# Performance work log

Hardware: AMD Instinct MI355X
Metric: run time of the kernel (lower is better)

Reference implementation:

```python
import jax, jax.numpy as jnp
import numpy as np

N_NODES = 100000
N_EDGES = 1600000
D_IN = 128
D_OUT = 128


def setup_inputs() -> dict:
    key = jax.random.key(0)
    k_x, k_s, k_r, k_w = jax.random.split(key, 4)
    x = jax.random.normal(k_x, (N_NODES, D_IN), dtype=jnp.float32)
    senders = jax.random.randint(k_s, (N_EDGES,), 0, N_NODES, dtype=jnp.int32)
    receivers = jax.random.randint(k_r, (N_EDGES,), 0, N_NODES, dtype=jnp.int32)
    # xavier_uniform for (D_IN, D_OUT)
    limit = float(np.sqrt(6.0 / (D_IN + D_OUT)))
    weight = jax.random.uniform(k_w, (D_IN, D_OUT), dtype=jnp.float32,
                                minval=-limit, maxval=limit)
    bias = jnp.zeros((D_OUT,), dtype=jnp.float32)
    return {"x": x, "senders": senders, "receivers": receivers,
            "n_node": N_NODES, "weight": weight, "bias": bias}


def reference(x, senders, receivers, n_node, weight, bias):
    # Linear node update: [N, D_in] @ [D_in, D_out] + bias
    h = jnp.dot(x, weight) + bias
    total_num_nodes = x.shape[0]

    # Degree counts via segment_sum of ones (symmetric normalization)
    ones = jnp.ones_like(senders)
    sender_degree = jax.ops.segment_sum(ones, senders, num_segments=total_num_nodes)
    receiver_degree = jax.ops.segment_sum(ones, receivers, num_segments=total_num_nodes)

    # Pre-scale by 1/sqrt(deg_out), scatter-sum along edges, post-scale by 1/sqrt(deg_in)
    h = h * jax.lax.rsqrt(jnp.maximum(sender_degree, 1.0))[:, None]
    agg = jax.ops.segment_sum(h[senders], receivers, num_segments=total_num_nodes)
    out = agg * jax.lax.rsqrt(jnp.maximum(receiver_degree, 1.0))[:, None]
    return out
```

## Files before the change

kernel.cpp:

```cpp
#include <hip/hip_runtime.h>
#include <hip/hip_bf16.h>
#include <stdint.h>

#define N_NODES 100000
#define N_EDGES 1600000
#define TILE 8192
#define NB 196
#define BIN_BLOCKS ((N_EDGES + TILE - 1) / TILE)

static const size_t OFF_H      = 0;
static const size_t OFF_SSCALE = 25600000;
static const size_t OFF_ROWP   = 26000000;
static const size_t OFF_RHIST  = 26400016;
static const size_t OFF_SHIST  = 26401040;
static const size_t OFF_RBASE  = 26402064;
static const size_t OFF_SBASE  = 26403088;
static const size_t OFF_RCUR   = 26404112;
static const size_t OFF_SCUR   = 26405136;
static const size_t OFF_EBUF   = 26406160;
static const size_t OFF_SBUF   = 32806160;

using short8 = __attribute__((ext_vector_type(8))) short;
using f32x4  = __attribute__((ext_vector_type(4))) float;

static __device__ __forceinline__ short f2bf(float f) {
    uint32_t u = __float_as_uint(f);
    uint32_t r = (u + 0x7fffu + ((u >> 16) & 1u)) >> 16;
    return (short)r;
}

__global__ __launch_bounds__(256) void hist196_kernel(const int* __restrict__ snd,
                                                      const int* __restrict__ rcv,
                                                      int* __restrict__ rhist,
                                                      int* __restrict__ shist) {
    __shared__ int hr[256], hs[256];
    int t = threadIdx.x;
    hr[t] = 0; hs[t] = 0;
    __syncthreads();
    int base = blockIdx.x * TILE;
    #pragma unroll
    for (int j = 0; j < 32; j++) {
        int idx = base + j * 256 + t;
        if (idx < N_EDGES) {
            atomicAdd(&hr[rcv[idx] >> 9], 1);
            atomicAdd(&hs[snd[idx] >> 9], 1);
        }
    }
    __syncthreads();
    if (t < NB) {
        if (hr[t]) atomicAdd(&rhist[t], hr[t]);
        if (hs[t]) atomicAdd(&shist[t], hs[t]);
    }
}

__global__ __launch_bounds__(256) void scanb_kernel(const int* __restrict__ rhist,
                                                    const int* __restrict__ shist,
                                                    int* __restrict__ rbase,
                                                    int* __restrict__ sbase,
                                                    int* __restrict__ rcur,
                                                    int* __restrict__ scur,
                                                    int* __restrict__ row_ptr) {
    __shared__ int s[256];
    int t = threadIdx.x;

    int v = (t < NB) ? rhist[t] : 0;
    s[t] = v;
    __syncthreads();
    #pragma unroll
    for (int off = 1; off < 256; off <<= 1) {
        int tv = (t >= off) ? s[t - off] : 0;
        __syncthreads();
        s[t] += tv;
        __syncthreads();
    }
    if (t < NB) { int e = s[t] - v; rbase[t] = e; rcur[t] = e; }
    __syncthreads();

    v = (t < NB) ? shist[t] : 0;
    s[t] = v;
    __syncthreads();
    #pragma unroll
    for (int off = 1; off < 256; off <<= 1) {
        int tv = (t >= off) ? s[t - off] : 0;
        __syncthreads();
        s[t] += tv;
        __syncthreads();
    }
    if (t < NB) { int e = s[t] - v; sbase[t] = e; scur[t] = e; }
    if (t == 0) row_ptr[N_NODES] = N_EDGES;
}

__global__ __launch_bounds__(256) void binr_kernel(const int* __restrict__ snd,
                                                   const int* __restrict__ rcv,
                                                   int* __restrict__ rcur,
                                                   int* __restrict__ scur,
                                                   uint32_t* __restrict__ ebuf,
                                                   uint16_t* __restrict__ sbuf) {
    __shared__ int hist[256];
    __shared__ int coff[256];
    __shared__ int ccur[256];
    __shared__ int gbase[256];
    __shared__ uint32_t stage[TILE];

    const int t = threadIdx.x;
    const int base = blockIdx.x * TILE;

    uint32_t ss[32], rs[32];
    #pragma unroll
    for (int j = 0; j < 32; j++) {
        int idx = base + j * 256 + t;
        bool ok = idx < N_EDGES;
        ss[j] = ok ? (uint32_t)snd[idx] : 0u;
        rs[j] = ok ? (uint32_t)rcv[idx] : 0xffffffffu;
    }

    hist[t] = 0;
    __syncthreads();
    #pragma unroll
    for (int j = 0; j < 32; j++)
        if (rs[j] != 0xffffffffu) atomicAdd(&hist[rs[j] >> 9], 1);
    __syncthreads();

    int v = hist[t];
    ccur[t] = v;
    __syncthreads();
    #pragma unroll
    for (int off = 1; off < 256; off <<= 1) {
        int tv = (t >= off) ? ccur[t - off] : 0;
        __syncthreads();
        ccur[t] += tv;
        __syncthreads();
    }
    int excl = ccur[t] - v;
    coff[t] = excl;
    int gb = 0;
    if (v > 0) gb = atomicAdd(&rcur[t], v);
    gbase[t] = gb - excl;
    __syncthreads();
    ccur[t] = excl;
    __syncthreads();

    #pragma unroll
    for (int j = 0; j < 32; j++) {
        uint32_t r = rs[j];
        if (r != 0xffffffffu) {
            int pos = atomicAdd(&ccur[r >> 9], 1);
            stage[pos] = (ss[j] << 9) | (r & 511u);
        }
    }
    __syncthreads();

    int total = coff[255] + hist[255];
    for (int i = t; i < total; i += 256) {
        uint32_t pv = stage[i];
        int lo = 0;
        #pragma unroll
        for (int step = 128; step; step >>= 1)
            if (lo + step < 256 && coff[lo + step] <= i) lo += step;
        ebuf[gbase[lo] + i] = pv;
    }
    __syncthreads();

    hist[t] = 0;
    __syncthreads();
    #pragma unroll
    for (int j = 0; j < 32; j++)
        if (rs[j] != 0xffffffffu) atomicAdd(&hist[ss[j] >> 9], 1);
    __syncthreads();

    v = hist[t];
    ccur[t] = v;
    __syncthreads();
    #pragma unroll
    for (int off = 1; off < 256; off <<= 1) {
        int tv = (t >= off) ? ccur[t - off] : 0;
        __syncthreads();
        ccur[t] += tv;
        __syncthreads();
    }
    excl = ccur[t] - v;
    coff[t] = excl;
    gb = 0;
    if (v > 0) gb = atomicAdd(&scur[t], v);
    gbase[t] = gb - excl;
    __syncthreads();
    ccur[t] = excl;
    __syncthreads();

    uint16_t* stage16 = (uint16_t*)stage;
    #pragma unroll
    for (int j = 0; j < 32; j++) {
        if (rs[j] != 0xffffffffu) {
            int pos = atomicAdd(&ccur[ss[j] >> 9], 1);
            stage16[pos] = (uint16_t)(ss[j] & 511u);
        }
    }
    __syncthreads();

    total = coff[255] + hist[255];
    for (int i = t; i < total; i += 256) {
        uint16_t pv = stage16[i];
        int lo = 0;
        #pragma unroll
        for (int step = 128; step; step >>= 1)
            if (lo + step < 256 && coff[lo + step] <= i) lo += step;
        sbuf[gbase[lo] + i] = pv;
    }
}

__global__ __launch_bounds__(256) void bucket_kernel(const int* __restrict__ rbase,
                                                     const int* __restrict__ rhist,
                                                     const int* __restrict__ sbase,
                                                     const int* __restrict__ shist,
                                                     uint32_t* __restrict__ ebuf,
                                                     const uint16_t* __restrict__ sbuf,
                                                     int* __restrict__ row_ptr,
                                                     float* __restrict__ sscale) {
    __shared__ int hist_l[512];
    __shared__ int excl_l[512];
    __shared__ int cur_l[512];
    __shared__ int ps[256];
    __shared__ uint32_t inb[9216];
    __shared__ uint32_t perm[9216];

    const int b = blockIdx.x;
    const int t = threadIdx.x;
    const int nbase = b << 9;
    const int base = rbase[b];
    const int size = rhist[b];

    hist_l[t] = 0; hist_l[t + 256] = 0;
    __syncthreads();

    for (int i = t; i < size; i += 256) {
        uint32_t v = ebuf[base + i];
        inb[i] = v;
        atomicAdd(&hist_l[v & 511u], 1);
    }
    __syncthreads();

    int h0 = hist_l[2 * t], h1 = hist_l[2 * t + 1];
    int p = h0 + h1;
    ps[t] = p;
    __syncthreads();
    #pragma unroll
    for (int off = 1; off < 256; off <<= 1) {
        int tv = (t >= off) ? ps[t - off] : 0;
        __syncthreads();
        ps[t] += tv;
        __syncthreads();
    }
    int pe = ps[t] - p;
    excl_l[2 * t] = pe;
    excl_l[2 * t + 1] = pe + h0;
    cur_l[2 * t] = pe;
    cur_l[2 * t + 1] = pe + h0;
    __syncthreads();

    for (int i = t; i < 512; i += 256) {
        int n = nbase + i;
        if (n < N_NODES) row_ptr[n] = base + excl_l[i];
    }

    for (int i = t; i < size; i += 256) {
        uint32_t v = inb[i];
        int pos = atomicAdd(&cur_l[v & 511u], 1);
        perm[pos] = v >> 9;
    }
    __syncthreads();
    for (int i = t; i < size; i += 256)
        ebuf[base + i] = perm[i];

    __syncthreads();
    hist_l[t] = 0; hist_l[t + 256] = 0;
    __syncthreads();
    const int sb = sbase[b];
    const int ssz = shist[b];
    for (int i = t; i < ssz; i += 256)
        atomicAdd(&hist_l[(int)sbuf[sb + i]], 1);
    __syncthreads();
    for (int i = t; i < 512; i += 256) {
        int n = nbase + i;
        if (n < N_NODES) sscale[n] = rsqrtf(fmaxf((float)hist_l[i], 1.f));
    }
}

__global__ __launch_bounds__(256) void gemm_mfma_kernel(const float* __restrict__ x,
                                                        const float* __restrict__ W,
                                                        const float* __restrict__ bias,
                                                        const float* __restrict__ sscale,
                                                        short* __restrict__ h) {
    __shared__ __align__(16) short Wl[32 * 64 * 8];
    __shared__ float bias_s[128];

    const int t = threadIdx.x;
    const int lane = t & 63;
    const int wv = t >> 6;
    const int quad = lane >> 4;
    const int mcol = lane & 15;

    #pragma unroll
    for (int i = 0; i < 8; i++) {
        int f = wv + 4 * i;
        int s = f >> 3;
        int c = f & 7;
        int krow = s * 32 + quad * 8;
        int ncol = c * 16 + mcol;
        short8 wf;
        #pragma unroll
        for (int j = 0; j < 8; j++)
            wf[j] = f2bf(W[(krow + j) * 128 + ncol]);
        *(short8*)&Wl[(f * 64 + lane) * 8] = wf;
    }
    if (t < 128) bias_s[t] = bias[t];

    const int node0 = blockIdx.x * 128 + wv * 32;
    short8 afrag[2][4];
    #pragma unroll
    for (int mf = 0; mf < 2; mf++) {
        int node = node0 + mf * 16 + mcol;
        bool ok = node < N_NODES;
        const float* xr = x + (size_t)(ok ? node : 0) * 128;
        #pragma unroll
        for (int s = 0; s < 4; s++) {
            int k0 = s * 32 + quad * 8;
            f32x4 v0 = ok ? *(const f32x4*)(xr + k0)     : f32x4{0.f,0.f,0.f,0.f};
            f32x4 v1 = ok ? *(const f32x4*)(xr + k0 + 4) : f32x4{0.f,0.f,0.f,0.f};
            short8 af;
            #pragma unroll
            for (int j = 0; j < 4; j++) {
                af[j]     = f2bf(v0[j]);
                af[4 + j] = f2bf(v1[j]);
            }
            afrag[mf][s] = af;
        }
    }

    __syncthreads();

    f32x4 acc[2][8];
    #pragma unroll
    for (int mf = 0; mf < 2; mf++)
        #pragma unroll
        for (int c = 0; c < 8; c++)
            acc[mf][c] = f32x4{0.f, 0.f, 0.f, 0.f};

    #pragma unroll
    for (int s = 0; s < 4; s++) {
        #pragma unroll
        for (int c = 0; c < 8; c++) {
            short8 bfrag = *(const short8*)&Wl[((s * 8 + c) * 64 + lane) * 8];
            acc[0][c] = __builtin_amdgcn_mfma_f32_16x16x32_bf16(afrag[0][s], bfrag, acc[0][c], 0, 0, 0);
            acc[1][c] = __builtin_amdgcn_mfma_f32_16x16x32_bf16(afrag[1][s], bfrag, acc[1][c], 0, 0, 0);
        }
    }

    float rsv[2][4];
    #pragma unroll
    for (int mf = 0; mf < 2; mf++)
        #pragma unroll
        for (int r = 0; r < 4; r++) {
            int nd = node0 + mf * 16 + quad * 4 + r;
            rsv[mf][r] = (nd < N_NODES) ? sscale[nd] : 1.f;
        }

    #pragma unroll
    for (int mf = 0; mf < 2; mf++)
        #pragma unroll
        for (int c = 0; c < 8; c++) {
            float bval = bias_s[c * 16 + mcol];
            #pragma unroll
            for (int r = 0; r < 4; r++) {
                int nd = node0 + mf * 16 + quad * 4 + r;
                if (nd < N_NODES)
                    h[(size_t)nd * 128 + c * 16 + mcol] =
                        f2bf((acc[mf][c][r] + bval) * rsv[mf][r]);
            }
        }
}

__global__ __launch_bounds__(256) void gather_kernel(const uint32_t* __restrict__ h2,
                                                     const int* __restrict__ row_ptr,
                                                     const uint32_t* __restrict__ esrc,
                                                     float2* __restrict__ out2) {
    int node = blockIdx.x * 4 + (threadIdx.x >> 6);
    int lane = threadIdx.x & 63;
    int b = row_ptr[node];
    int e = row_ptr[node + 1];
    float a0 = 0.f, a1 = 0.f;
    int i = b;
    for (; i + 4 <= e; i += 4) {
        uint32_t s0 = esrc[i + 0], s1 = esrc[i + 1], s2 = esrc[i + 2], s3 = esrc[i + 3];
        uint32_t v0 = h2[(size_t)s0 * 64 + lane];
        uint32_t v1 = h2[(size_t)s1 * 64 + lane];
        uint32_t v2 = h2[(size_t)s2 * 64 + lane];
        uint32_t v3 = h2[(size_t)s3 * 64 + lane];
        a0 += __uint_as_float(v0 << 16) + __uint_as_float(v1 << 16)
            + __uint_as_float(v2 << 16) + __uint_as_float(v3 << 16);
        a1 += __uint_as_float(v0 & 0xffff0000u) + __uint_as_float(v1 & 0xffff0000u)
            + __uint_as_float(v2 & 0xffff0000u) + __uint_as_float(v3 & 0xffff0000u);
    }
    for (; i < e; i++) {
        uint32_t s = esrc[i];
        uint32_t v = h2[(size_t)s * 64 + lane];
        a0 += __uint_as_float(v << 16);
        a1 += __uint_as_float(v & 0xffff0000u);
    }
    float rs = rsqrtf(fmaxf((float)(e - b), 1.f));
    out2[(size_t)node * 64 + lane] = make_float2(a0 * rs, a1 * rs);
}

extern "C" void kernel_launch(void* const* d_in, const int* in_sizes, int n_in,
                              void* d_out, int out_size, void* d_ws, size_t ws_size,
                              hipStream_t stream) {
    const float* x    = (const float*)d_in[0];
    const int*   snd  = (const int*)d_in[1];
    const int*   rcv  = (const int*)d_in[2];
    const float* W    = (const float*)d_in[4];
    const float* bias = (const float*)d_in[5];

    char* ws = (char*)d_ws;
    short*    h      = (short*)(ws + OFF_H);
    float*    sscale = (float*)(ws + OFF_SSCALE);
    int*      rowp   = (int*)(ws + OFF_ROWP);
    int*      rhist  = (int*)(ws + OFF_RHIST);
    int*      shist  = (int*)(ws + OFF_SHIST);
    int*      rbase  = (int*)(ws + OFF_RBASE);
    int*      sbase  = (int*)(ws + OFF_SBASE);
    int*      rcur   = (int*)(ws + OFF_RCUR);
    int*      scur   = (int*)(ws + OFF_SCUR);
    uint32_t* ebuf   = (uint32_t*)(ws + OFF_EBUF);
    uint16_t* sbuf   = (uint16_t*)(ws + OFF_SBUF);

    hipMemsetAsync(ws + OFF_RHIST, 0, 2048, stream);

    hist196_kernel <<<BIN_BLOCKS, 256, 0, stream>>>(snd, rcv, rhist, shist);
    scanb_kernel   <<<1, 256, 0, stream>>>(rhist, shist, rbase, sbase, rcur, scur, rowp);
    binr_kernel    <<<BIN_BLOCKS, 256, 0, stream>>>(snd, rcv, rcur, scur, ebuf, sbuf);
    bucket_kernel  <<<NB, 256, 0, stream>>>(rbase, rhist, sbase, shist, ebuf, sbuf, rowp, sscale);
    gemm_mfma_kernel<<<(N_NODES + 127) / 128, 256, 0, stream>>>(x, W, bias, sscale, h);
    gather_kernel  <<<N_NODES / 4, 256, 0, stream>>>((const uint32_t*)h, rowp, ebuf, (float2*)d_out);
}
```

Before: 275.8 us.

## Precompute bf16 weight fragments once and widen gather to half-wave per node

Adds a small prep kernel that converts W to bf16 MFMA fragments once, so each GEMM block reads the fragments directly from global memory instead of converting and staging W in LDS. This also removes the LDS buffer and the barrier, and sets an occupancy hint on the GEMM. The gather kernel now gives each node half a wave, with each lane loading 8 bytes and writing a float4, which halves the block count and widens the memory accesses. The trade-off is an extra kernel launch and per-block global/L2 reads of the fragments instead of LDS reads.

```diff
diff --git a/kernel.cpp b/kernel.cpp
--- a/kernel.cpp
+++ b/kernel.cpp
@@ -17,8 +17,9 @@
 static const size_t OFF_SBASE  = 26403088;
 static const size_t OFF_RCUR   = 26404112;
 static const size_t OFF_SCUR   = 26405136;
-static const size_t OFF_EBUF   = 26406160;
-static const size_t OFF_SBUF   = 32806160;
+static const size_t OFF_WFRAG  = 26406160;
+static const size_t OFF_EBUF   = 26438928;
+static const size_t OFF_SBUF   = 32838928;
 
 using short8 = __attribute__((ext_vector_type(8))) short;
 using f32x4  = __attribute__((ext_vector_type(4))) float;
@@ -27,6 +28,21 @@
     uint32_t u = __float_as_uint(f);
     uint32_t r = (u + 0x7fffu + ((u >> 16) & 1u)) >> 16;
     return (short)r;
+}
+
+__global__ __launch_bounds__(256) void prep_w_kernel(const float* __restrict__ W,
+                                                     short8* __restrict__ wfrag) {
+    int slot = blockIdx.x * 256 + threadIdx.x;
+    int f = slot >> 6, lane = slot & 63;
+    int quad = lane >> 4, mcol = lane & 15;
+    int s = f >> 3, c = f & 7;
+    int krow = s * 32 + quad * 8;
+    int ncol = c * 16 + mcol;
+    short8 wf;
+    #pragma unroll
+    for (int j = 0; j < 8; j++)
+        wf[j] = f2bf(W[(krow + j) * 128 + ncol]);
+    wfrag[slot] = wf;
 }
 
 __global__ __launch_bounds__(256) void hist196_kernel(const int* __restrict__ snd,
@@ -285,34 +301,16 @@
     }
 }
 
-__global__ __launch_bounds__(256) void gemm_mfma_kernel(const float* __restrict__ x,
-                                                        const float* __restrict__ W,
-                                                        const float* __restrict__ bias,
-                                                        const float* __restrict__ sscale,
-                                                        short* __restrict__ h) {
-    __shared__ __align__(16) short Wl[32 * 64 * 8];
-    __shared__ float bias_s[128];
-
+__global__ __launch_bounds__(256, 3) void gemm_mfma_kernel(const float* __restrict__ x,
+                                                           const short8* __restrict__ wfrag,
+                                                           const float* __restrict__ bias,
+                                                           const float* __restrict__ sscale,
+                                                           short* __restrict__ h) {
     const int t = threadIdx.x;
     const int lane = t & 63;
     const int wv = t >> 6;
     const int quad = lane >> 4;
     const int mcol = lane & 15;
-
-    #pragma unroll
-    for (int i = 0; i < 8; i++) {
-        int f = wv + 4 * i;
-        int s = f >> 3;
-        int c = f & 7;
-        int krow = s * 32 + quad * 8;
-        int ncol = c * 16 + mcol;
-        short8 wf;
-        #pragma unroll
-        for (int j = 0; j < 8; j++)
-            wf[j] = f2bf(W[(krow + j) * 128 + ncol]);
-        *(short8*)&Wl[(f * 64 + lane) * 8] = wf;
-    }
-    if (t < 128) bias_s[t] = bias[t];
 
     const int node0 = blockIdx.x * 128 + wv * 32;
     short8 afrag[2][4];
@@ -336,8 +334,6 @@
         }
     }
 
-    __syncthreads();
-
     f32x4 acc[2][8];
     #pragma unroll
     for (int mf = 0; mf < 2; mf++)
@@ -349,7 +345,7 @@
     for (int s = 0; s < 4; s++) {
         #pragma unroll
         for (int c = 0; c < 8; c++) {
-            short8 bfrag = *(const short8*)&Wl[((s * 8 + c) * 64 + lane) * 8];
+            short8 bfrag = wfrag[(s * 8 + c) * 64 + lane];
             acc[0][c] = __builtin_amdgcn_mfma_f32_16x16x32_bf16(afrag[0][s], bfrag, acc[0][c], 0, 0, 0);
             acc[1][c] = __builtin_amdgcn_mfma_f32_16x16x32_bf16(afrag[1][s], bfrag, acc[1][c], 0, 0, 0);
         }
@@ -368,7 +364,7 @@
     for (int mf = 0; mf < 2; mf++)
         #pragma unroll
         for (int c = 0; c < 8; c++) {
-            float bval = bias_s[c * 16 + mcol];
+            float bval = bias[c * 16 + mcol];
             #pragma unroll
             for (int r = 0; r < 4; r++) {
                 int nd = node0 + mf * 16 + quad * 4 + r;
@@ -382,32 +378,42 @@
 __global__ __launch_bounds__(256) void gather_kernel(const uint32_t* __restrict__ h2,
                                                      const int* __restrict__ row_ptr,
                                                      const uint32_t* __restrict__ esrc,
-                                                     float2* __restrict__ out2) {
-    int node = blockIdx.x * 4 + (threadIdx.x >> 6);
+                                                     float4* __restrict__ out4) {
+    int wv = threadIdx.x >> 6;
     int lane = threadIdx.x & 63;
+    int half = lane >> 5;
+    int ln = lane & 31;
+    int node = blockIdx.x * 8 + wv * 2 + half;
+
     int b = row_ptr[node];
     int e = row_ptr[node + 1];
-    float a0 = 0.f, a1 = 0.f;
+    float a0 = 0.f, a1 = 0.f, a2 = 0.f, a3 = 0.f;
     int i = b;
     for (; i + 4 <= e; i += 4) {
         uint32_t s0 = esrc[i + 0], s1 = esrc[i + 1], s2 = esrc[i + 2], s3 = esrc[i + 3];
-        uint32_t v0 = h2[(size_t)s0 * 64 + lane];
-        uint32_t v1 = h2[(size_t)s1 * 64 + lane];
-        uint32_t v2 = h2[(size_t)s2 * 64 + lane];
-        uint32_t v3 = h2[(size_t)s3 * 64 + lane];
-        a0 += __uint_as_float(v0 << 16) + __uint_as_float(v1 << 16)
-            + __uint_as_float(v2 << 16) + __uint_as_float(v3 << 16);
-        a1 += __uint_as_float(v0 & 0xffff0000u) + __uint_as_float(v1 & 0xffff0000u)
-            + __uint_as_float(v2 & 0xffff0000u) + __uint_as_float(v3 & 0xffff0000u);
+        uint2 v0 = *(const uint2*)&h2[(size_t)s0 * 64 + ln * 2];
+        uint2 v1 = *(const uint2*)&h2[(size_t)s1 * 64 + ln * 2];
+        uint2 v2 = *(const uint2*)&h2[(size_t)s2 * 64 + ln * 2];
+        uint2 v3 = *(const uint2*)&h2[(size_t)s3 * 64 + ln * 2];
+        a0 += __uint_as_float(v0.x << 16) + __uint_as_float(v1.x << 16)
+            + __uint_as_float(v2.x << 16) + __uint_as_float(v3.x << 16);
+        a1 += __uint_as_float(v0.x & 0xffff0000u) + __uint_as_float(v1.x & 0xffff0000u)
+            + __uint_as_float(v2.x & 0xffff0000u) + __uint_as_float(v3.x & 0xffff0000u);
+        a2 += __uint_as_float(v0.y << 16) + __uint_as_float(v1.y << 16)
+            + __uint_as_float(v2.y << 16) + __uint_as_float(v3.y << 16);
+        a3 += __uint_as_float(v0.y & 0xffff0000u) + __uint_as_float(v1.y & 0xffff0000u)
+            + __uint_as_float(v2.y & 0xffff0000u) + __uint_as_float(v3.y & 0xffff0000u);
     }
     for (; i < e; i++) {
         uint32_t s = esrc[i];
-        uint32_t v = h2[(size_t)s * 64 + lane];
-        a0 += __uint_as_float(v << 16);
-        a1 += __uint_as_float(v & 0xffff0000u);
+        uint2 v = *(const uint2*)&h2[(size_t)s * 64 + ln * 2];
+        a0 += __uint_as_float(v.x << 16);
+        a1 += __uint_as_float(v.x & 0xffff0000u);
+        a2 += __uint_as_float(v.y << 16);
+        a3 += __uint_as_float(v.y & 0xffff0000u);
     }
     float rs = rsqrtf(fmaxf((float)(e - b), 1.f));
-    out2[(size_t)node * 64 + lane] = make_float2(a0 * rs, a1 * rs);
+    out4[(size_t)node * 32 + ln] = make_float4(a0 * rs, a1 * rs, a2 * rs, a3 * rs);
 }
 
 extern "C" void kernel_launch(void* const* d_in, const int* in_sizes, int n_in,
@@ -429,15 +435,17 @@
     int*      sbase  = (int*)(ws + OFF_SBASE);
     int*      rcur   = (int*)(ws + OFF_RCUR);
     int*      scur   = (int*)(ws + OFF_SCUR);
+    short8*   wfrag  = (short8*)(ws + OFF_WFRAG);
     uint32_t* ebuf   = (uint32_t*)(ws + OFF_EBUF);
     uint16_t* sbuf   = (uint16_t*)(ws + OFF_SBUF);
 
     hipMemsetAsync(ws + OFF_RHIST, 0, 2048, stream);
 
+    prep_w_kernel  <<<8, 256, 0, stream>>>(W, wfrag);
     hist196_kernel <<<BIN_BLOCKS, 256, 0, stream>>>(snd, rcv, rhist, shist);
     scanb_kernel   <<<1, 256, 0, stream>>>(rhist, shist, rbase, sbase, rcur, scur, rowp);
     binr_kernel    <<<BIN_BLOCKS, 256, 0, stream>>>(snd, rcv, rcur, scur, ebuf, sbuf);
     bucket_kernel  <<<NB, 256, 0, stream>>>(rbase, rhist, sbase, shist, ebuf, sbuf, rowp, sscale);
-    gemm_mfma_kernel<<<(N_NODES + 127) / 128, 256, 0, stream>>>(x, W, bias, sscale, h);
-    gather_kernel  <<<N_NODES / 4, 256, 0, stream>>>((const uint32_t*)h, rowp, ebuf, (float2*)d_out);
-}
+    gemm_mfma_kernel<<<(N_NODES + 127) / 128, 256, 0, stream>>>(x, wfrag, bias, sscale, h);
+    gather_kernel  <<<N_NODES / 8, 256, 0, stream>>>((const uint32_t*)h, rowp, ebuf, (float4*)d_out);
+}
```

Result: no change. 272.3 us (-1.3%).
